# Performance work log

Measured on AMD Instinct MI355X. Metric: run time of the kernel, lower is better.

Reference implementation:

```python
import jax, jax.numpy as jnp
import numpy as np

IN_DIM = 1024
HEAD_DIM = 64
NUM_HEADS = 16
SEQ = 4096


def setup_inputs() -> dict:
    key = jax.random.key(0)
    ks = jax.random.split(key, 7)
    s = 1.0 / np.sqrt(IN_DIM)
    return {
        "h": jax.random.normal(ks[0], (SEQ, IN_DIM), dtype=jnp.float32),
        "Wq": jax.random.uniform(ks[1], (IN_DIM, NUM_HEADS * HEAD_DIM), jnp.float32, -s, s),
        "Wk": jax.random.uniform(ks[2], (IN_DIM, NUM_HEADS * HEAD_DIM), jnp.float32, -s, s),
        "Wv": jax.random.uniform(ks[3], (IN_DIM, NUM_HEADS * HEAD_DIM), jnp.float32, -s, s),
        "bq": jax.random.uniform(ks[4], (NUM_HEADS * HEAD_DIM,), jnp.float32, -s, s),
        "bk": jax.random.uniform(ks[5], (NUM_HEADS * HEAD_DIM,), jnp.float32, -s, s),
        "bv": jax.random.uniform(ks[6], (NUM_HEADS * HEAD_DIM,), jnp.float32, -s, s),
    }


def reference(h, Wq, Wk, Wv, bq, bk, bv):
    n = h.shape[0]
    # QKV projections -> [H, S, D]
    q = (h @ Wq + bq).reshape(n, NUM_HEADS, HEAD_DIM).transpose(1, 0, 2)
    k = (h @ Wk + bk).reshape(n, NUM_HEADS, HEAD_DIM).transpose(1, 0, 2)
    v = (h @ Wv + bv).reshape(n, NUM_HEADS, HEAD_DIM).transpose(1, 0, 2)
    scale = 1.0 / np.sqrt(HEAD_DIM).astype(np.float32)
    scores = jnp.einsum('hsd,htd->hst', q, k) * scale  # [H, S, S]
    probs = jax.nn.softmax(scores, axis=-1)
    out = jnp.einsum('hst,htd->hsd', probs, v)  # [H, S, D]
    return out.transpose(1, 0, 2).reshape(n, NUM_HEADS * HEAD_DIM)
```

## Files before the change

### kernel.cpp

```cpp
#include <hip/hip_runtime.h>
#include <hip/hip_bf16.h>

#define IN_DIM    1024
#define HEAD_DIM  64
#define NUM_HEADS 16
#define SEQ       4096

#define QSCALE 0.125f

typedef __bf16 bf16;
typedef __attribute__((ext_vector_type(4))) __bf16 bf16x4;
typedef __attribute__((ext_vector_type(8))) __bf16 bf16x8;
typedef __attribute__((ext_vector_type(4))) float floatx4;

__device__ __forceinline__ void async16(bf16* lds, const bf16* g) {
    __builtin_amdgcn_global_load_lds(
        (const __attribute__((address_space(1))) unsigned int*)g,
        (__attribute__((address_space(3))) unsigned int*)lds, 16, 0, 0);
}


__global__ void mha_conv_h(const float* __restrict__ h, bf16* __restrict__ hb) {
    int i = blockIdx.x * blockDim.x + threadIdx.x;
    float4 v = ((const float4*)h)[i];
    bf16x4 r;
    r[0] = (bf16)v.x; r[1] = (bf16)v.y; r[2] = (bf16)v.z; r[3] = (bf16)v.w;
    ((bf16x4*)hb)[i] = r;
}

__global__ void mha_conv_wt(const float* __restrict__ Wq, const float* __restrict__ Wk,
                            const float* __restrict__ Wv, bf16* __restrict__ Wt) {
    __shared__ bf16 tile[64][65];
    const int mat = blockIdx.z;
    const float* W = (mat == 0) ? Wq : (mat == 1) ? Wk : Wv;
    const int k0 = blockIdx.y * 64, n0 = blockIdx.x * 64;
    const int tn = threadIdx.x & 63, tq = threadIdx.x >> 6;
#pragma unroll
    for (int i = 0; i < 16; ++i) {
        int kk = tq + i * 4;
        tile[kk][tn] = (bf16)W[(size_t)(k0 + kk) * 1024 + n0 + tn];
    }
    __syncthreads();
#pragma unroll
    for (int i = 0; i < 16; ++i) {
        int nn = tq + i * 4;
        Wt[((size_t)mat << 20) + (size_t)(n0 + nn) * 1024 + k0 + tn] = tile[tn][nn];
    }
}

__launch_bounds__(256)
__global__ void mha_qkv_gemm(const bf16* __restrict__ hb, const bf16* __restrict__ Wt,
                             const float* __restrict__ bq, const float* __restrict__ bk,
                             const float* __restrict__ bv,
                             bf16* __restrict__ Qb, bf16* __restrict__ Kb,
                             bf16* __restrict__ Vt) {
    __shared__ __align__(16) bf16 As[128 * 32];
    __shared__ __align__(16) bf16 Bs[128 * 32];

    const int lane = threadIdx.x & 63;
    const int wave = threadIdx.x >> 6;
    const int l16  = lane & 15;
    const int quad = lane >> 4;
    const int wm   = wave & 1;
    const int wn   = wave >> 1;

    const int m0  = blockIdx.x * 128;
    const int n0  = blockIdx.y * 128;
    const int mat = n0 >> 10;
    const int nc0 = n0 & 1023;

    const bf16* Wp = Wt + ((size_t)mat << 20);

    floatx4 acc[4][4] = {};
    const int swz = (l16 >> 1) & 3;

    for (int k0 = 0; k0 < IN_DIM; k0 += 32) {
#pragma unroll
        for (int r = 0; r < 2; ++r) {
            int g = wave * 128 + r * 64 + lane;
            int row = g >> 2, c = g & 3;
            int gc = c ^ ((row >> 1) & 3);
            bf16* ldsbase_a = As + (size_t)(wave * 128 + r * 64) * 8;
            bf16* ldsbase_b = Bs + (size_t)(wave * 128 + r * 64) * 8;
            async16(ldsbase_a, hb + (size_t)(m0 + row) * IN_DIM + k0 + gc * 8);
            async16(ldsbase_b, Wp + (size_t)(nc0 + row) * IN_DIM + k0 + gc * 8);
        }
        __syncthreads();

        bf16x8 af[4], bf[4];
#pragma unroll
        for (int mt = 0; mt < 4; ++mt)
            af[mt] = *(const bf16x8*)(As + (size_t)(wm * 64 + mt * 16 + l16) * 32
                                      + ((quad ^ swz) * 8));
#pragma unroll
        for (int nt = 0; nt < 4; ++nt)
            bf[nt] = *(const bf16x8*)(Bs + (size_t)(wn * 64 + nt * 16 + l16) * 32
                                      + ((quad ^ swz) * 8));
#pragma unroll
        for (int mt = 0; mt < 4; ++mt)
#pragma unroll
            for (int nt = 0; nt < 4; ++nt)
                acc[mt][nt] = __builtin_amdgcn_mfma_f32_16x16x32_bf16(af[mt], bf[nt],
                                                                      acc[mt][nt], 0, 0, 0);
        __syncthreads();
    }

    const float* bias = (mat == 0) ? bq : (mat == 1) ? bk : bv;
#pragma unroll
    for (int nt = 0; nt < 4; ++nt) {
        int nc = nc0 + wn * 64 + nt * 16 + l16;
        float bb = bias[nc];
        int head = nc >> 6, d = nc & 63;
#pragma unroll
        for (int mt = 0; mt < 4; ++mt)
#pragma unroll
            for (int r = 0; r < 4; ++r) {
                int srow = m0 + wm * 64 + mt * 16 + quad * 4 + r;
                float v = acc[mt][nt][r] + bb;
                if (mat == 0)
                    Qb[((size_t)head * SEQ + srow) * HEAD_DIM + d] = (bf16)(v * QSCALE);
                else if (mat == 1)
                    Kb[((size_t)head * SEQ + srow) * HEAD_DIM + d] = (bf16)v;
                else
                    Vt[((size_t)head * HEAD_DIM + d) * SEQ + srow] = (bf16)v;
            }
    }
}

__launch_bounds__(256)
__global__ void mha_attn(const bf16* __restrict__ Qb, const bf16* __restrict__ Kb,
                         const bf16* __restrict__ Vt, float* __restrict__ out) {
    __shared__ __align__(16) bf16 Ks[2][64 * 64];
    __shared__ __align__(16) bf16 Vs[2][64 * 64];
    __shared__ __align__(16) bf16 Ps[4][2][16 * 72];

    const int lane = threadIdx.x & 63;
    const int wave = threadIdx.x >> 6;
    const int l16  = lane & 15;
    const int quad = lane >> 4;

    const int hh    = blockIdx.y;
    const int qbase = blockIdx.x * 128 + wave * 32;

    const bf16* Qh = Qb + (size_t)hh * SEQ * HEAD_DIM;
    const bf16* Kh = Kb + (size_t)hh * SEQ * HEAD_DIM;
    const bf16* Vh = Vt + (size_t)hh * HEAD_DIM * SEQ;

    const int sg   = wave * 128 + lane;
    const int ldsb = wave * 128;

    bf16x8 qf[2][2];
#pragma unroll
    for (int mt = 0; mt < 2; ++mt)
#pragma unroll
        for (int ks = 0; ks < 2; ++ks)
            qf[mt][ks] = *(const bf16x8*)(Qh + (size_t)(qbase + mt * 16 + l16) * HEAD_DIM
                                          + ks * 32 + quad * 8);

    bf16x8 vone;
#pragma unroll
    for (int i = 0; i < 8; ++i) vone[i] = (bf16)1.0f;

    floatx4 o[2][4] = {};
    floatx4 ol[2]   = {};

    bf16* lp0 = &Ps[wave][0][0];
    bf16* lp1 = &Ps[wave][1][0];
    const int swk = l16 & 7;

#pragma unroll
    for (int r = 0; r < 2; ++r) {
        int g = sg + r * 64, row = g >> 3, gc = (g & 7) ^ (row & 7);
        async16(&Ks[0][(ldsb + r * 64) * 8], Kh + (size_t)row * HEAD_DIM + gc * 8);
        async16(&Vs[0][(ldsb + r * 64) * 8], Vh + (size_t)row * SEQ + gc * 8);
    }
    __syncthreads();

    for (int t0 = 0; t0 < SEQ; t0 += 64) {
        const int cur = (t0 >> 6) & 1, nxt = cur ^ 1;
        if (t0 + 64 < SEQ) {
#pragma unroll
            for (int r = 0; r < 2; ++r) {
                int g = sg + r * 64, row = g >> 3, gc = (g & 7) ^ (row & 7);
                async16(&Ks[nxt][(ldsb + r * 64) * 8],
                        Kh + (size_t)(t0 + 64 + row) * HEAD_DIM + gc * 8);
                async16(&Vs[nxt][(ldsb + r * 64) * 8],
                        Vh + (size_t)row * SEQ + t0 + 64 + gc * 8);
            }
        }

        bf16x8 kf[4][2], vf[4][2];
#pragma unroll
        for (int tt = 0; tt < 4; ++tt)
#pragma unroll
            for (int ks = 0; ks < 2; ++ks)
                kf[tt][ks] = *(const bf16x8*)(&Ks[cur][(size_t)(tt * 16 + l16) * 64
                                              + (((ks * 4 + quad) ^ swk) * 8)]);
#pragma unroll
        for (int dt = 0; dt < 4; ++dt)
#pragma unroll
            for (int ks = 0; ks < 2; ++ks)
                vf[dt][ks] = *(const bf16x8*)(&Vs[cur][(size_t)(dt * 16 + l16) * 64
                                              + (((ks * 4 + quad) ^ swk) * 8)]);

#pragma unroll
        for (int mt = 0; mt < 2; ++mt) {
            bf16* lp = mt ? lp1 : lp0;
#pragma unroll
            for (int tt = 0; tt < 4; ++tt) {
                floatx4 s = {};
                s = __builtin_amdgcn_mfma_f32_16x16x32_bf16(kf[tt][0], qf[mt][0], s, 0, 0, 0);
                s = __builtin_amdgcn_mfma_f32_16x16x32_bf16(kf[tt][1], qf[mt][1], s, 0, 0, 0);
                bf16x4 pk;
#pragma unroll
                for (int r = 0; r < 4; ++r) pk[r] = (bf16)__expf(s[r]);
                *(bf16x4*)(lp + l16 * 72 + tt * 16 + quad * 4) = pk;
            }
        }

#pragma unroll
        for (int mt = 0; mt < 2; ++mt) {
            bf16* lp = mt ? lp1 : lp0;
#pragma unroll
            for (int ks = 0; ks < 2; ++ks) {
                bf16x8 pf = *(const bf16x8*)(lp + l16 * 72 + ks * 32 + quad * 8);
#pragma unroll
                for (int dt = 0; dt < 4; ++dt)
                    o[mt][dt] = __builtin_amdgcn_mfma_f32_16x16x32_bf16(pf, vf[dt][ks],
                                                                        o[mt][dt], 0, 0, 0);
                ol[mt] = __builtin_amdgcn_mfma_f32_16x16x32_bf16(pf, vone, ol[mt], 0, 0, 0);
            }
        }
        __syncthreads();
    }

#pragma unroll
    for (int mt = 0; mt < 2; ++mt)
#pragma unroll
        for (int r = 0; r < 4; ++r) {
            float inv = 1.0f / ol[mt][r];
            int srow = qbase + mt * 16 + quad * 4 + r;
#pragma unroll
            for (int dt = 0; dt < 4; ++dt)
                out[(size_t)srow * (NUM_HEADS * HEAD_DIM) + hh * 64 + dt * 16 + l16]
                    = o[mt][dt][r] * inv;
        }
}

extern "C" void kernel_launch(void* const* d_in, const int* in_sizes, int n_in,
                              void* d_out, int out_size, void* d_ws, size_t ws_size,
                              hipStream_t stream) {
    const float* h  = (const float*)d_in[0];
    const float* Wq = (const float*)d_in[1];
    const float* Wk = (const float*)d_in[2];
    const float* Wv = (const float*)d_in[3];
    const float* bq = (const float*)d_in[4];
    const float* bk = (const float*)d_in[5];
    const float* bv = (const float*)d_in[6];
    float* out = (float*)d_out;

    char* ws = (char*)d_ws;
    const size_t MB = 1024 * 1024;
    bf16* hb = (bf16*)(ws);
    bf16* Wt = (bf16*)(ws + 8 * MB);
    bf16* Qb = (bf16*)(ws + 14 * MB);
    bf16* Kb = (bf16*)(ws + 22 * MB);
    bf16* Vt = (bf16*)(ws + 30 * MB);

    mha_conv_h<<<(SEQ * IN_DIM / 4) / 256, 256, 0, stream>>>(h, hb);
    mha_conv_wt<<<dim3(16, 16, 3), 256, 0, stream>>>(Wq, Wk, Wv, Wt);
    mha_qkv_gemm<<<dim3(SEQ / 128, (3 * IN_DIM) / 128), 256, 0, stream>>>(
        hb, Wt, bq, bk, bv, Qb, Kb, Vt);
    mha_attn<<<dim3(SEQ / 128, NUM_HEADS), 256, 0, stream>>>(Qb, Kb, Vt, out);
}
```

Before: 215.2 us.

## Use 8 waves of 16 query rows per attention block and exp2 softmax

The attention kernel now launches 512 threads per block. Each of 8 waves handles 16 query rows instead of 4 waves handling 32, so each K/V tile in LDS is shared by more waves and per-wave register pressure drops. The Q scale absorbs log2(e) so the softmax exponent can use the hardware exp2 instead of __expf. The trade-off is more MFMA loads of K/V fragments per unit of work, since each wave reloads all K/V fragments for only 16 rows, and more barrier participants.

```diff
diff --git a/kernel.cpp b/kernel.cpp
--- a/kernel.cpp
+++ b/kernel.cpp
@@ -6,7 +6,7 @@
 #define NUM_HEADS 16
 #define SEQ       4096
 
-#define QSCALE 0.125f
+#define QSCALE 0.18033688011112042f
 
 typedef __bf16 bf16;
 typedef __attribute__((ext_vector_type(4))) __bf16 bf16x4;
@@ -127,12 +127,12 @@
     }
 }
 
-__launch_bounds__(256)
+__launch_bounds__(512)
 __global__ void mha_attn(const bf16* __restrict__ Qb, const bf16* __restrict__ Kb,
                          const bf16* __restrict__ Vt, float* __restrict__ out) {
     __shared__ __align__(16) bf16 Ks[2][64 * 64];
     __shared__ __align__(16) bf16 Vs[2][64 * 64];
-    __shared__ __align__(16) bf16 Ps[4][2][16 * 72];
+    __shared__ __align__(16) bf16 Ps[8][16 * 72];
 
     const int lane = threadIdx.x & 63;
     const int wave = threadIdx.x >> 6;
@@ -140,53 +140,40 @@
     const int quad = lane >> 4;
 
     const int hh    = blockIdx.y;
-    const int qbase = blockIdx.x * 128 + wave * 32;
+    const int qbase = blockIdx.x * 128 + wave * 16;
 
     const bf16* Qh = Qb + (size_t)hh * SEQ * HEAD_DIM;
     const bf16* Kh = Kb + (size_t)hh * SEQ * HEAD_DIM;
     const bf16* Vh = Vt + (size_t)hh * HEAD_DIM * SEQ;
 
-    const int sg   = wave * 128 + lane;
-    const int ldsb = wave * 128;
-
-    bf16x8 qf[2][2];
-#pragma unroll
-    for (int mt = 0; mt < 2; ++mt)
-#pragma unroll
-        for (int ks = 0; ks < 2; ++ks)
-            qf[mt][ks] = *(const bf16x8*)(Qh + (size_t)(qbase + mt * 16 + l16) * HEAD_DIM
-                                          + ks * 32 + quad * 8);
+    const int sg   = wave * 64 + lane;
+    const int srow = sg >> 3;
+    const int sgc  = (sg & 7) ^ (srow & 7);
+
+    bf16x8 qf[2];
+#pragma unroll
+    for (int ks = 0; ks < 2; ++ks)
+        qf[ks] = *(const bf16x8*)(Qh + (size_t)(qbase + l16) * HEAD_DIM + ks * 32 + quad * 8);
 
     bf16x8 vone;
 #pragma unroll
     for (int i = 0; i < 8; ++i) vone[i] = (bf16)1.0f;
 
-    floatx4 o[2][4] = {};
-    floatx4 ol[2]   = {};
-
-    bf16* lp0 = &Ps[wave][0][0];
-    bf16* lp1 = &Ps[wave][1][0];
+    floatx4 o[4] = {};
+    floatx4 ol   = {};
+
+    bf16* lp = &Ps[wave][0];
     const int swk = l16 & 7;
 
-#pragma unroll
-    for (int r = 0; r < 2; ++r) {
-        int g = sg + r * 64, row = g >> 3, gc = (g & 7) ^ (row & 7);
-        async16(&Ks[0][(ldsb + r * 64) * 8], Kh + (size_t)row * HEAD_DIM + gc * 8);
-        async16(&Vs[0][(ldsb + r * 64) * 8], Vh + (size_t)row * SEQ + gc * 8);
-    }
+    async16(&Ks[0][wave * 512], Kh + (size_t)srow * HEAD_DIM + sgc * 8);
+    async16(&Vs[0][wave * 512], Vh + (size_t)srow * SEQ + sgc * 8);
     __syncthreads();
 
     for (int t0 = 0; t0 < SEQ; t0 += 64) {
         const int cur = (t0 >> 6) & 1, nxt = cur ^ 1;
         if (t0 + 64 < SEQ) {
-#pragma unroll
-            for (int r = 0; r < 2; ++r) {
-                int g = sg + r * 64, row = g >> 3, gc = (g & 7) ^ (row & 7);
-                async16(&Ks[nxt][(ldsb + r * 64) * 8],
-                        Kh + (size_t)(t0 + 64 + row) * HEAD_DIM + gc * 8);
-                async16(&Vs[nxt][(ldsb + r * 64) * 8],
-                        Vh + (size_t)row * SEQ + t0 + 64 + gc * 8);
-            }
+            async16(&Ks[nxt][wave * 512], Kh + (size_t)(t0 + 64 + srow) * HEAD_DIM + sgc * 8);
+            async16(&Vs[nxt][wave * 512], Vh + (size_t)srow * SEQ + t0 + 64 + sgc * 8);
         }
 
         bf16x8 kf[4][2], vf[4][2];
@@ -204,47 +191,36 @@
                                               + (((ks * 4 + quad) ^ swk) * 8)]);
 
 #pragma unroll
-        for (int mt = 0; mt < 2; ++mt) {
-            bf16* lp = mt ? lp1 : lp0;
-#pragma unroll
-            for (int tt = 0; tt < 4; ++tt) {
-                floatx4 s = {};
-                s = __builtin_amdgcn_mfma_f32_16x16x32_bf16(kf[tt][0], qf[mt][0], s, 0, 0, 0);
-                s = __builtin_amdgcn_mfma_f32_16x16x32_bf16(kf[tt][1], qf[mt][1], s, 0, 0, 0);
-                bf16x4 pk;
-#pragma unroll
-                for (int r = 0; r < 4; ++r) pk[r] = (bf16)__expf(s[r]);
-                *(bf16x4*)(lp + l16 * 72 + tt * 16 + quad * 4) = pk;
-            }
-        }
-
-#pragma unroll
-        for (int mt = 0; mt < 2; ++mt) {
-            bf16* lp = mt ? lp1 : lp0;
-#pragma unroll
-            for (int ks = 0; ks < 2; ++ks) {
-                bf16x8 pf = *(const bf16x8*)(lp + l16 * 72 + ks * 32 + quad * 8);
-#pragma unroll
-                for (int dt = 0; dt < 4; ++dt)
-                    o[mt][dt] = __builtin_amdgcn_mfma_f32_16x16x32_bf16(pf, vf[dt][ks],
-                                                                        o[mt][dt], 0, 0, 0);
-                ol[mt] = __builtin_amdgcn_mfma_f32_16x16x32_bf16(pf, vone, ol[mt], 0, 0, 0);
-            }
+        for (int tt = 0; tt < 4; ++tt) {
+            floatx4 s = {};
+            s = __builtin_amdgcn_mfma_f32_16x16x32_bf16(kf[tt][0], qf[0], s, 0, 0, 0);
+            s = __builtin_amdgcn_mfma_f32_16x16x32_bf16(kf[tt][1], qf[1], s, 0, 0, 0);
+            bf16x4 pk;
+#pragma unroll
+            for (int r = 0; r < 4; ++r) pk[r] = (bf16)__builtin_amdgcn_exp2f(s[r]);
+            *(bf16x4*)(lp + l16 * 72 + tt * 16 + quad * 4) = pk;
+        }
+
+#pragma unroll
+        for (int ks = 0; ks < 2; ++ks) {
+            bf16x8 pf = *(const bf16x8*)(lp + l16 * 72 + ks * 32 + quad * 8);
+#pragma unroll
+            for (int dt = 0; dt < 4; ++dt)
+                o[dt] = __builtin_amdgcn_mfma_f32_16x16x32_bf16(pf, vf[dt][ks], o[dt], 0, 0, 0);
+            ol = __builtin_amdgcn_mfma_f32_16x16x32_bf16(pf, vone, ol, 0, 0, 0);
         }
         __syncthreads();
     }
 
 #pragma unroll
-    for (int mt = 0; mt < 2; ++mt)
-#pragma unroll
-        for (int r = 0; r < 4; ++r) {
-            float inv = 1.0f / ol[mt][r];
-            int srow = qbase + mt * 16 + quad * 4 + r;
-#pragma unroll
-            for (int dt = 0; dt < 4; ++dt)
-                out[(size_t)srow * (NUM_HEADS * HEAD_DIM) + hh * 64 + dt * 16 + l16]
-                    = o[mt][dt][r] * inv;
-        }
+    for (int r = 0; r < 4; ++r) {
+        float inv = 1.0f / ol[r];
+        int srow_o = qbase + quad * 4 + r;
+#pragma unroll
+        for (int dt = 0; dt < 4; ++dt)
+            out[(size_t)srow_o * (NUM_HEADS * HEAD_DIM) + hh * 64 + dt * 16 + l16]
+                = o[dt][r] * inv;
+    }
 }
 
 extern "C" void kernel_launch(void* const* d_in, const int* in_sizes, int n_in,
@@ -271,5 +247,5 @@
     mha_conv_wt<<<dim3(16, 16, 3), 256, 0, stream>>>(Wq, Wk, Wv, Wt);
     mha_qkv_gemm<<<dim3(SEQ / 128, (3 * IN_DIM) / 128), 256, 0, stream>>>(
         hb, Wt, bq, bk, bv, Qb, Kb, Vt);
-    mha_attn<<<dim3(SEQ / 128, NUM_HEADS), 256, 0, stream>>>(Qb, Kb, Vt, out);
-}
+    mha_attn<<<dim3(SEQ / 128, NUM_HEADS), 512, 0, stream>>>(Qb, Kb, Vt, out);
+}
```

Measured after the change: 204.2 us. 5.1% less time.
